# Performance work log

Measured on AMD Instinct MI355X. Metric: run time of the kernel, lower is better.

The kernel has to match this reference:

```python
import jax, jax.numpy as jnp
import numpy as np
import math

# kinematic tree: parent of each of the 23 joints (parents[i] < i -> topological order)
PARENTS = np.array([-1, 0, 1, 1, 3, 4, 5, 4, 7, 4, 9, 1, 11, 12, 13, 12, 15, 12, 17, 0, 19, 0, 21])
NUM_J = 23
HALF, QUART = math.pi / 2.0, math.pi / 4.0
# (joint slot, scale) for the pose params actually written in the torch forward
POSE_SLOTS = [(0, QUART), (3, HALF), (4, HALF), (5, QUART), (7, QUART), (9, QUART),
              (11, HALF), (12, HALF), (13, QUART), (15, QUART), (17, QUART)]


def _rodrigues(r):
    # r: [..., 3] axis-angle -> [..., 3, 3] rotation matrix
    angle = jnp.sqrt(jnp.sum(r * r, axis=-1) + 1e-16)
    axis = r / angle[..., None]
    s, c = jnp.sin(angle), jnp.cos(angle)
    x, y, z = axis[..., 0], axis[..., 1], axis[..., 2]
    zero = jnp.zeros_like(x)
    K = jnp.stack([jnp.stack([zero, -z, y], -1),
                   jnp.stack([z, zero, -x], -1),
                   jnp.stack([-y, x, zero], -1)], -2)
    I = jnp.eye(3, dtype=r.dtype)
    return I + s[..., None, None] * K + (1.0 - c)[..., None, None] * (K @ K)


def _lbs_forward(vertices, joints, weights, displacement, random_dis, pose_params):
    P = displacement.shape[0]
    dt = vertices.dtype
    # per-joint pose: pi/4 or pi/2 * tanh(param) on the used slots, zeros elsewhere
    pose = jnp.zeros((P, NUM_J, 3), dt)
    for (idx, scale), prm in zip(POSE_SLOTS, pose_params):
        pose = pose.at[:, idx].set(scale * jnp.tanh(prm))
    R = _rodrigues(pose)                                          # [P,J,3,3]
    j = joints[0].astype(dt)                                      # [J,3] rest joints
    rel = jnp.concatenate([j[:1], j[1:] - j[PARENTS[1:]]], 0)     # joint offsets from parent
    top = jnp.concatenate([R, jnp.broadcast_to(rel[None, :, :, None], (P, NUM_J, 3, 1))], -1)
    bot = jnp.broadcast_to(jnp.array([0.0, 0.0, 0.0, 1.0], dt), (P, NUM_J, 1, 4))
    T_local = jnp.concatenate([top, bot], -2)                     # [P,J,4,4]
    # forward-kinematics tree walk (fixed 23-joint chain, parents precede children)
    Gs = [T_local[:, 0]]
    for i in range(1, NUM_J):
        Gs.append(Gs[PARENTS[i]] @ T_local[:, i])
    G = jnp.stack(Gs, 1)                                          # [P,J,4,4]
    posed_joints = G[..., :3, 3]                                  # [P,J,3]
    # A = G - [0 | G_rot @ j_rest]  (keep only the 3x4 part actually needed)
    A = G[:, :, :3, :].at[..., 3].add(-jnp.einsum('pjab,jb->pja', G[:, :, :3, :3], j))  # [P,J,3,4]
    W = weights.astype(dt)
    T = jnp.einsum('vj,pjab->pvab', W, A)                         # [P,V,3,4] skinning transforms
    v = vertices[0]                                               # [V,3]
    v_posed = jnp.einsum('pvij,vj->pvi', T[..., :3], v) + T[..., 3]  # [P,V,3]
    shift = random_dis[:, None, :] + 3.0 * jnp.tanh(displacement)   # [P,1,3]
    return v_posed + shift, posed_joints + shift


def setup_inputs():
    P, V, J = 16, 500000, NUM_J
    key = jax.random.key(0)
    ks = jax.random.split(key, 16)
    w = jax.random.uniform(ks[2], (V, J), jnp.float32)
    inp = {
        'vertices': jax.random.normal(ks[0], (1, V, 3), jnp.float32),
        'joints': jax.random.normal(ks[1], (1, J, 3), jnp.float32),
        'weights': w / jnp.sum(w, -1, keepdims=True),  # convex skinning weights
        'displacement': 0.1 * jax.random.normal(ks[3], (P, 1, 3), jnp.float32),
        'random_dis': jax.random.normal(ks[4], (P, 3), jnp.float32),
    }
    names = ['joint_0', 'joint_3', 'joint_4', 'joint_5', 'joint_7', 'joint_9',
             'joint_11', 'joint_12', 'joint_13', 'joint_15', 'joint_17']
    for i, n in enumerate(names):
        inp[n] = jax.random.normal(ks[5 + i], (P, 3), jnp.float32)
    return inp


def reference(vertices, joints, weights, displacement, random_dis, joint_0, joint_3, joint_4, joint_5, joint_7, joint_9, joint_11, joint_12, joint_13, joint_15, joint_17):
    pose_params = (joint_0, joint_3, joint_4, joint_5, joint_7, joint_9,
                   joint_11, joint_12, joint_13, joint_15, joint_17)
    return _lbs_forward(vertices, joints, weights, displacement, random_dis, pose_params)
```

## Files before the change

### kernel.cpp

```cpp
#include <hip/hip_runtime.h>
#include <hip/hip_bf16.h>

typedef __hip_bfloat16 bf16;

#define P_CNT 16
#define J_CNT 23

__device__ int    g_flag;
__device__ float4 g_A[P_CNT * J_CNT * 3];
__device__ float  g_shift[P_CNT * 3];

struct PosePtrs { const void* p[11]; };

template <bool BF>
__device__ __forceinline__ float ld(const void* p, long long i) {
    if (BF) return __bfloat162float(((const bf16*)p)[i]);
    return ((const float*)p)[i];
}
template <bool BF>
__device__ __forceinline__ void st(void* p, long long i, float v) {
    if (BF) ((bf16*)p)[i] = __float2bfloat16(v);
    else    ((float*)p)[i] = v;
}

__global__ void detect_kernel(const void* __restrict__ w) {
    if (threadIdx.x != 0 || blockIdx.x != 0) return;
    const float* wf = (const float*)w;
    const bf16*  wb = (const bf16*)w;
    bool ok_f = true, ok_b = true;
    for (int r = 0; r < 4; ++r) {
        float sf = 0.f, sb = 0.f;
        for (int j = 0; j < J_CNT; ++j) {
            sf += wf[r * J_CNT + j];
            sb += __bfloat162float(wb[r * J_CNT + j]);
        }
        if (!(fabsf(sf - 1.f) < 0.02f)) ok_f = false;
        if (!(fabsf(sb - 1.f) < 0.10f)) ok_b = false;
    }
    g_flag = (!ok_f && ok_b) ? 1 : 0;
}

template <bool BF>
__global__ void pose_kernel(const void* __restrict__ joints,
                            const void* __restrict__ disp,
                            const void* __restrict__ rdis,
                            PosePtrs pp,
                            void* __restrict__ out1)
{
    if (g_flag != (BF ? 1 : 0)) return;
    __shared__ float Gs[P_CNT][J_CNT][12];
    int p = threadIdx.x;
    if (p >= P_CNT) return;

    const int par[J_CNT]     = {-1,0,1,1,3,4,5,4,7,4,9,1,11,12,13,12,15,12,17,0,19,0,21};
    const int slot_of[J_CNT] = {0,-1,-1,1,2,3,-1,4,-1,5,-1,6,7,8,-1,9,-1,10,-1,-1,-1,-1,-1};
    const float slot_sc[11]  = {
        0.7853981633974483f, 1.5707963267948966f, 1.5707963267948966f, 0.7853981633974483f,
        0.7853981633974483f, 0.7853981633974483f, 1.5707963267948966f, 1.5707963267948966f,
        0.7853981633974483f, 0.7853981633974483f, 0.7853981633974483f};

    for (int j = 0; j < J_CNT; ++j) {
        float rx = 0.f, ry = 0.f, rz = 0.f;
        int s = slot_of[j];
        if (s >= 0) {
            float sc = slot_sc[s];
            rx = sc * tanhf(ld<BF>(pp.p[s], p * 3 + 0));
            ry = sc * tanhf(ld<BF>(pp.p[s], p * 3 + 1));
            rz = sc * tanhf(ld<BF>(pp.p[s], p * 3 + 2));
        }
        float ang = sqrtf(rx * rx + ry * ry + rz * rz + 1e-16f);
        float sn = sinf(ang), cs = cosf(ang);
        float C = 1.f - cs;
        float inva = 1.f / ang;
        float x = rx * inva, y = ry * inva, z = rz * inva;
        float R[3][3];
        R[0][0] = 1.f - C * (y * y + z * z); R[0][1] = -sn * z + C * x * y;       R[0][2] = sn * y + C * x * z;
        R[1][0] = sn * z + C * x * y;        R[1][1] = 1.f - C * (x * x + z * z); R[1][2] = -sn * x + C * y * z;
        R[2][0] = -sn * y + C * x * z;       R[2][1] = sn * x + C * y * z;        R[2][2] = 1.f - C * (x * x + y * y);

        int q = par[j];
        float t[3];
        for (int c = 0; c < 3; ++c) {
            float jc = ld<BF>(joints, j * 3 + c);
            t[c] = (j == 0) ? jc : (jc - ld<BF>(joints, q * 3 + c));
        }
        if (j == 0) {
            for (int i = 0; i < 3; ++i) {
                Gs[p][0][i * 4 + 0] = R[i][0];
                Gs[p][0][i * 4 + 1] = R[i][1];
                Gs[p][0][i * 4 + 2] = R[i][2];
                Gs[p][0][i * 4 + 3] = t[i];
            }
        } else {
            for (int i = 0; i < 3; ++i) {
                float g0 = Gs[p][q][i * 4 + 0], g1 = Gs[p][q][i * 4 + 1];
                float g2 = Gs[p][q][i * 4 + 2], g3 = Gs[p][q][i * 4 + 3];
                Gs[p][j][i * 4 + 0] = g0 * R[0][0] + g1 * R[1][0] + g2 * R[2][0];
                Gs[p][j][i * 4 + 1] = g0 * R[0][1] + g1 * R[1][1] + g2 * R[2][1];
                Gs[p][j][i * 4 + 2] = g0 * R[0][2] + g1 * R[1][2] + g2 * R[2][2];
                Gs[p][j][i * 4 + 3] = g0 * t[0] + g1 * t[1] + g2 * t[2] + g3;
            }
        }
    }

    float sh[3];
    for (int c = 0; c < 3; ++c) {
        sh[c] = ld<BF>(rdis, p * 3 + c) + 3.f * tanhf(ld<BF>(disp, p * 3 + c));
        g_shift[p * 3 + c] = sh[c];
    }

    for (int j = 0; j < J_CNT; ++j) {
        float jx = ld<BF>(joints, j * 3 + 0);
        float jy = ld<BF>(joints, j * 3 + 1);
        float jz = ld<BF>(joints, j * 3 + 2);
        for (int i = 0; i < 3; ++i) {
            float g0 = Gs[p][j][i * 4 + 0], g1 = Gs[p][j][i * 4 + 1];
            float g2 = Gs[p][j][i * 4 + 2], g3 = Gs[p][j][i * 4 + 3];
            g_A[(p * J_CNT + j) * 3 + i] =
                make_float4(g0, g1, g2, g3 - (g0 * jx + g1 * jy + g2 * jz));
            st<BF>(out1, (p * J_CNT + j) * 3 + i, g3 + sh[i]);
        }
    }
}

template <bool BF>
__global__ __launch_bounds__(256) void lbs_vertex(
    const void* __restrict__ verts,
    const void* __restrict__ weights,
    void* __restrict__ out0,
    int V)
{
    if (g_flag != (BF ? 1 : 0)) return;
    __shared__ float4 As[P_CNT * J_CNT * 3];
    __shared__ float  sh[P_CNT * 3];
    for (int i = threadIdx.x; i < P_CNT * J_CNT * 3; i += 256) As[i] = g_A[i];
    for (int i = threadIdx.x; i < P_CNT * 3; i += 256) sh[i] = g_shift[i];
    __syncthreads();

    int v = blockIdx.x * 256 + threadIdx.x;
    if (v >= V) return;

    float w[J_CNT];
    long long wbase = (long long)v * J_CNT;
#pragma unroll
    for (int j = 0; j < J_CNT; ++j) w[j] = ld<BF>(weights, wbase + j);
    float x = ld<BF>(verts, (long long)v * 3 + 0);
    float y = ld<BF>(verts, (long long)v * 3 + 1);
    float z = ld<BF>(verts, (long long)v * 3 + 2);

    for (int p = 0; p < P_CNT; ++p) {
        const float4* Ap = As + p * (J_CNT * 3);
        float4 t0 = make_float4(0.f, 0.f, 0.f, 0.f);
        float4 t1 = make_float4(0.f, 0.f, 0.f, 0.f);
        float4 t2 = make_float4(0.f, 0.f, 0.f, 0.f);
#pragma unroll
        for (int j = 0; j < J_CNT; ++j) {
            float wj = w[j];
            float4 a0 = Ap[j * 3 + 0], a1 = Ap[j * 3 + 1], a2 = Ap[j * 3 + 2];
            t0.x = fmaf(wj, a0.x, t0.x); t0.y = fmaf(wj, a0.y, t0.y);
            t0.z = fmaf(wj, a0.z, t0.z); t0.w = fmaf(wj, a0.w, t0.w);
            t1.x = fmaf(wj, a1.x, t1.x); t1.y = fmaf(wj, a1.y, t1.y);
            t1.z = fmaf(wj, a1.z, t1.z); t1.w = fmaf(wj, a1.w, t1.w);
            t2.x = fmaf(wj, a2.x, t2.x); t2.y = fmaf(wj, a2.y, t2.y);
            t2.z = fmaf(wj, a2.z, t2.z); t2.w = fmaf(wj, a2.w, t2.w);
        }
        float ox = fmaf(t0.x, x, fmaf(t0.y, y, fmaf(t0.z, z, t0.w))) + sh[p * 3 + 0];
        float oy = fmaf(t1.x, x, fmaf(t1.y, y, fmaf(t1.z, z, t1.w))) + sh[p * 3 + 1];
        float oz = fmaf(t2.x, x, fmaf(t2.y, y, fmaf(t2.z, z, t2.w))) + sh[p * 3 + 2];
        long long base = ((long long)p * V + v) * 3;
        st<BF>(out0, base + 0, ox);
        st<BF>(out0, base + 1, oy);
        st<BF>(out0, base + 2, oz);
    }
}

extern "C" void kernel_launch(void* const* d_in, const int* in_sizes, int n_in,
                              void* d_out, int out_size, void* d_ws, size_t ws_size,
                              hipStream_t stream) {
    const void* verts   = d_in[0];
    const void* joints  = d_in[1];
    const void* weights = d_in[2];
    const void* disp    = d_in[3];
    const void* rdis    = d_in[4];
    PosePtrs pp;
    for (int i = 0; i < 11; ++i) pp.p[i] = d_in[5 + i];

    int V = in_sizes[0] / 3;
    long long pv3 = (long long)P_CNT * V * 3;

    void* out1_f = (void*)((float*)d_out + pv3);
    void* out1_b = (void*)((bf16*) d_out + pv3);

    detect_kernel<<<1, 64, 0, stream>>>(weights);
    pose_kernel<false><<<1, 64, 0, stream>>>(joints, disp, rdis, pp, out1_f);
    pose_kernel<true ><<<1, 64, 0, stream>>>(joints, disp, rdis, pp, out1_b);
    int G = (V + 255) / 256;
    lbs_vertex<false><<<G, 256, 0, stream>>>(verts, weights, d_out, V);
    lbs_vertex<true ><<<G, 256, 0, stream>>>(verts, weights, d_out, V);
}
```

Measured before the change: 253.6 us.

## Fuse pose, detection and skinning into one kernel with register-tiled vertices

Replaces the five-launch pipeline (dtype detection, two pose kernels, two vertex kernels) with a single kernel. Each block recomputes the forward-kinematics transforms in shared memory, stages a tile of skinning weights in shared memory with a swizzled transposed layout, and has each thread handle one pose and 16 vertices using vectorized loads and stores. This removes the launch overhead and the global round-trip for transforms. In exchange every block redundantly recomputes the tiny pose chain on 16 threads, and the kernel uses much more shared memory and registers.

```diff
diff --git a/kernel.cpp b/kernel.cpp
--- a/kernel.cpp
+++ b/kernel.cpp
@@ -5,12 +5,18 @@
 
 #define P_CNT 16
 #define J_CNT 23
-
-__device__ int    g_flag;
-__device__ float4 g_A[P_CNT * J_CNT * 3];
-__device__ float  g_shift[P_CNT * 3];
+#define VB    256
+#define VPT   16
+#define WSTR  260
 
 struct PosePtrs { const void* p[11]; };
+
+__device__ const int   c_par[J_CNT]  = {-1,0,1,1,3,4,5,4,7,4,9,1,11,12,13,12,15,12,17,0,19,0,21};
+__device__ const int   c_slot[J_CNT] = {0,-1,-1,1,2,3,-1,4,-1,5,-1,6,7,8,-1,9,-1,10,-1,-1,-1,-1,-1};
+__device__ const float c_scale[11]   = {
+    0.7853981633974483f, 1.5707963267948966f, 1.5707963267948966f, 0.7853981633974483f,
+    0.7853981633974483f, 0.7853981633974483f, 1.5707963267948966f, 1.5707963267948966f,
+    0.7853981633974483f, 0.7853981633974483f, 0.7853981633974483f};
 
 template <bool BF>
 __device__ __forceinline__ float ld(const void* p, long long i) {
@@ -22,156 +28,258 @@
     if (BF) ((bf16*)p)[i] = __float2bfloat16(v);
     else    ((float*)p)[i] = v;
 }
-
-__global__ void detect_kernel(const void* __restrict__ w) {
-    if (threadIdx.x != 0 || blockIdx.x != 0) return;
-    const float* wf = (const float*)w;
-    const bf16*  wb = (const bf16*)w;
-    bool ok_f = true, ok_b = true;
-    for (int r = 0; r < 4; ++r) {
-        float sf = 0.f, sb = 0.f;
+__device__ __forceinline__ float bfu(unsigned short u) {
+    union { unsigned short s; bf16 h; } c; c.s = u; return __bfloat162float(c.h);
+}
+__device__ __forceinline__ unsigned pack_bf(float a, float b) {
+    union { bf16 h; unsigned short u; } A, B;
+    A.h = __float2bfloat16(a); B.h = __float2bfloat16(b);
+    return ((unsigned)B.u << 16) | (unsigned)A.u;
+}
+
+template <bool BF>
+__device__ __forceinline__ void run(const void* __restrict__ verts,
+                                    const void* __restrict__ joints,
+                                    const void* __restrict__ weights,
+                                    const void* __restrict__ disp,
+                                    const void* __restrict__ rdis,
+                                    const PosePtrs& pp,
+                                    void* __restrict__ out, int V,
+                                    float* sA, float* sW, float* sSh)
+{
+    const int t = threadIdx.x;
+    const long long vb = (long long)blockIdx.x * VB;
+
+    {
+        const long long totalF = (long long)V * J_CNT;
+        const long long baseF  = vb * J_CNT;
+#pragma unroll 1
+        for (int e = t; e < VB * J_CNT; e += 256) {
+            float val = (baseF + e < totalF) ? ld<BF>(weights, baseF + e) : 0.f;
+            int r  = e / J_CNT;
+            int j  = e - r * J_CNT;
+            int wr = r ^ (((r >> 4) & 7) << 2);
+            sW[j * WSTR + wr] = val;
+        }
+    }
+
+    if (t < P_CNT) {
+        const int p = t;
+        float* Gp = sA + p * (J_CNT * 12);
+#pragma unroll 1
         for (int j = 0; j < J_CNT; ++j) {
-            sf += wf[r * J_CNT + j];
-            sb += __bfloat162float(wb[r * J_CNT + j]);
-        }
-        if (!(fabsf(sf - 1.f) < 0.02f)) ok_f = false;
-        if (!(fabsf(sb - 1.f) < 0.10f)) ok_b = false;
-    }
-    g_flag = (!ok_f && ok_b) ? 1 : 0;
-}
-
-template <bool BF>
-__global__ void pose_kernel(const void* __restrict__ joints,
-                            const void* __restrict__ disp,
-                            const void* __restrict__ rdis,
-                            PosePtrs pp,
-                            void* __restrict__ out1)
-{
-    if (g_flag != (BF ? 1 : 0)) return;
-    __shared__ float Gs[P_CNT][J_CNT][12];
-    int p = threadIdx.x;
-    if (p >= P_CNT) return;
-
-    const int par[J_CNT]     = {-1,0,1,1,3,4,5,4,7,4,9,1,11,12,13,12,15,12,17,0,19,0,21};
-    const int slot_of[J_CNT] = {0,-1,-1,1,2,3,-1,4,-1,5,-1,6,7,8,-1,9,-1,10,-1,-1,-1,-1,-1};
-    const float slot_sc[11]  = {
-        0.7853981633974483f, 1.5707963267948966f, 1.5707963267948966f, 0.7853981633974483f,
-        0.7853981633974483f, 0.7853981633974483f, 1.5707963267948966f, 1.5707963267948966f,
-        0.7853981633974483f, 0.7853981633974483f, 0.7853981633974483f};
-
+            float rx = 0.f, ry = 0.f, rz = 0.f;
+            int s = c_slot[j];
+            if (s >= 0) {
+                float sc = c_scale[s];
+                rx = sc * tanhf(ld<BF>(pp.p[s], p * 3 + 0));
+                ry = sc * tanhf(ld<BF>(pp.p[s], p * 3 + 1));
+                rz = sc * tanhf(ld<BF>(pp.p[s], p * 3 + 2));
+            }
+            float ang = sqrtf(rx * rx + ry * ry + rz * rz + 1e-16f);
+            float sn = sinf(ang), cs = cosf(ang);
+            float C = 1.f - cs, inva = 1.f / ang;
+            float x = rx * inva, y = ry * inva, z = rz * inva;
+            float R00 = 1.f - C * (y * y + z * z), R01 = -sn * z + C * x * y, R02 = sn * y + C * x * z;
+            float R10 = sn * z + C * x * y, R11 = 1.f - C * (x * x + z * z), R12 = -sn * x + C * y * z;
+            float R20 = -sn * y + C * x * z, R21 = sn * x + C * y * z, R22 = 1.f - C * (x * x + y * y);
+            int q = c_par[j];
+            float t0 = ld<BF>(joints, j * 3 + 0);
+            float t1 = ld<BF>(joints, j * 3 + 1);
+            float t2 = ld<BF>(joints, j * 3 + 2);
+            if (j == 0) {
+                Gp[0] = R00; Gp[1] = R01; Gp[2]  = R02; Gp[3]  = t0;
+                Gp[4] = R10; Gp[5] = R11; Gp[6]  = R12; Gp[7]  = t1;
+                Gp[8] = R20; Gp[9] = R21; Gp[10] = R22; Gp[11] = t2;
+            } else {
+                t0 -= ld<BF>(joints, q * 3 + 0);
+                t1 -= ld<BF>(joints, q * 3 + 1);
+                t2 -= ld<BF>(joints, q * 3 + 2);
+                const float* Gq = Gp + q * 12;
+                float* Gj = Gp + j * 12;
+#pragma unroll
+                for (int i = 0; i < 3; ++i) {
+                    float g0 = Gq[i * 4 + 0], g1 = Gq[i * 4 + 1];
+                    float g2 = Gq[i * 4 + 2], g3 = Gq[i * 4 + 3];
+                    Gj[i * 4 + 0] = g0 * R00 + g1 * R10 + g2 * R20;
+                    Gj[i * 4 + 1] = g0 * R01 + g1 * R11 + g2 * R21;
+                    Gj[i * 4 + 2] = g0 * R02 + g1 * R12 + g2 * R22;
+                    Gj[i * 4 + 3] = g0 * t0 + g1 * t1 + g2 * t2 + g3;
+                }
+            }
+        }
+#pragma unroll
+        for (int cc = 0; cc < 3; ++cc)
+            sSh[t * 3 + cc] = ld<BF>(rdis, t * 3 + cc) + 3.f * tanhf(ld<BF>(disp, t * 3 + cc));
+    }
+    __syncthreads();
+
+    {
+        const long long pv3 = (long long)P_CNT * V * 3;
+        void* out1 = BF ? (void*)((bf16*)out + pv3) : (void*)((float*)out + pv3);
+#pragma unroll 1
+        for (int idx = t; idx < P_CNT * J_CNT; idx += 256) {
+            int p = idx / J_CNT;
+            int j = idx - p * J_CNT;
+            float jx = ld<BF>(joints, j * 3 + 0);
+            float jy = ld<BF>(joints, j * 3 + 1);
+            float jz = ld<BF>(joints, j * 3 + 2);
+            float* Ar = sA + (p * J_CNT + j) * 12;
+#pragma unroll
+            for (int i = 0; i < 3; ++i) {
+                float g0 = Ar[i * 4 + 0], g1 = Ar[i * 4 + 1];
+                float g2 = Ar[i * 4 + 2], g3 = Ar[i * 4 + 3];
+                Ar[i * 4 + 3] = g3 - (g0 * jx + g1 * jy + g2 * jz);
+                if (blockIdx.x == 0)
+                    st<BF>(out1, (long long)(p * J_CNT + j) * 3 + i, g3 + sSh[p * 3 + i]);
+            }
+        }
+    }
+
+    const int p = t >> 4, c = t & 15;
+    const long long v0 = vb + (long long)c * VPT;
+    const bool full = (v0 + VPT <= (long long)V);
+    union F48 { float4 q[12]; float s[48]; };
+    F48 P3;
+    if (!BF && full) {
+        const float4* vp = (const float4*)((const float*)verts + v0 * 3);
+#pragma unroll
+        for (int k = 0; k < 12; ++k) P3.q[k] = vp[k];
+    } else if (BF && full) {
+        const uint4* vp = (const uint4*)((const bf16*)verts + v0 * 3);
+#pragma unroll
+        for (int k = 0; k < 6; ++k) {
+            uint4 u = vp[k];
+            P3.s[k * 8 + 0] = bfu((unsigned short)(u.x & 0xffff));
+            P3.s[k * 8 + 1] = bfu((unsigned short)(u.x >> 16));
+            P3.s[k * 8 + 2] = bfu((unsigned short)(u.y & 0xffff));
+            P3.s[k * 8 + 3] = bfu((unsigned short)(u.y >> 16));
+            P3.s[k * 8 + 4] = bfu((unsigned short)(u.z & 0xffff));
+            P3.s[k * 8 + 5] = bfu((unsigned short)(u.z >> 16));
+            P3.s[k * 8 + 6] = bfu((unsigned short)(u.w & 0xffff));
+            P3.s[k * 8 + 7] = bfu((unsigned short)(u.w >> 16));
+        }
+    } else {
+        const long long lim = (long long)V * 3;
+#pragma unroll
+        for (int i = 0; i < 48; ++i) {
+            long long gi = v0 * 3 + i;
+            P3.s[i] = (gi < lim) ? ld<BF>(verts, gi) : 0.f;
+        }
+    }
+    __syncthreads();
+
+    float acc0[VPT], acc1[VPT], acc2[VPT];
+#pragma unroll
+    for (int v = 0; v < VPT; ++v) { acc0[v] = 0.f; acc1[v] = 0.f; acc2[v] = 0.f; }
+
+    const int xm  = (c & 7) << 2;
+    const int wq0 = (c * 16 + 0)  ^ xm;
+    const int wq1 = (c * 16 + 4)  ^ xm;
+    const int wq2 = (c * 16 + 8)  ^ xm;
+    const int wq3 = (c * 16 + 12) ^ xm;
+    const float* Ap = sA + p * (J_CNT * 12);
+
+#pragma unroll 1
     for (int j = 0; j < J_CNT; ++j) {
-        float rx = 0.f, ry = 0.f, rz = 0.f;
-        int s = slot_of[j];
-        if (s >= 0) {
-            float sc = slot_sc[s];
-            rx = sc * tanhf(ld<BF>(pp.p[s], p * 3 + 0));
-            ry = sc * tanhf(ld<BF>(pp.p[s], p * 3 + 1));
-            rz = sc * tanhf(ld<BF>(pp.p[s], p * 3 + 2));
-        }
-        float ang = sqrtf(rx * rx + ry * ry + rz * rz + 1e-16f);
-        float sn = sinf(ang), cs = cosf(ang);
-        float C = 1.f - cs;
-        float inva = 1.f / ang;
-        float x = rx * inva, y = ry * inva, z = rz * inva;
-        float R[3][3];
-        R[0][0] = 1.f - C * (y * y + z * z); R[0][1] = -sn * z + C * x * y;       R[0][2] = sn * y + C * x * z;
-        R[1][0] = sn * z + C * x * y;        R[1][1] = 1.f - C * (x * x + z * z); R[1][2] = -sn * x + C * y * z;
-        R[2][0] = -sn * y + C * x * z;       R[2][1] = sn * x + C * y * z;        R[2][2] = 1.f - C * (x * x + y * y);
-
-        int q = par[j];
-        float t[3];
-        for (int c = 0; c < 3; ++c) {
-            float jc = ld<BF>(joints, j * 3 + c);
-            t[c] = (j == 0) ? jc : (jc - ld<BF>(joints, q * 3 + c));
-        }
-        if (j == 0) {
-            for (int i = 0; i < 3; ++i) {
-                Gs[p][0][i * 4 + 0] = R[i][0];
-                Gs[p][0][i * 4 + 1] = R[i][1];
-                Gs[p][0][i * 4 + 2] = R[i][2];
-                Gs[p][0][i * 4 + 3] = t[i];
-            }
+        float4 a0 = *(const float4*)(Ap + j * 12 + 0);
+        float4 a1 = *(const float4*)(Ap + j * 12 + 4);
+        float4 a2 = *(const float4*)(Ap + j * 12 + 8);
+        const float* Wj = sW + j * WSTR;
+        union { float4 q[4]; float s[16]; } W;
+        W.q[0] = *(const float4*)(Wj + wq0);
+        W.q[1] = *(const float4*)(Wj + wq1);
+        W.q[2] = *(const float4*)(Wj + wq2);
+        W.q[3] = *(const float4*)(Wj + wq3);
+#pragma unroll
+        for (int v = 0; v < VPT; ++v) {
+            float x = P3.s[v * 3 + 0], y = P3.s[v * 3 + 1], z = P3.s[v * 3 + 2];
+            float wv = W.s[v];
+            float d0 = fmaf(a0.z, z, fmaf(a0.y, y, fmaf(a0.x, x, a0.w)));
+            float d1 = fmaf(a1.z, z, fmaf(a1.y, y, fmaf(a1.x, x, a1.w)));
+            float d2 = fmaf(a2.z, z, fmaf(a2.y, y, fmaf(a2.x, x, a2.w)));
+            acc0[v] = fmaf(wv, d0, acc0[v]);
+            acc1[v] = fmaf(wv, d1, acc1[v]);
+            acc2[v] = fmaf(wv, d2, acc2[v]);
+        }
+    }
+
+    const float shx = sSh[p * 3 + 0], shy = sSh[p * 3 + 1], shz = sSh[p * 3 + 2];
+    F48 O;
+#pragma unroll
+    for (int v = 0; v < VPT; ++v) {
+        O.s[v * 3 + 0] = acc0[v] + shx;
+        O.s[v * 3 + 1] = acc1[v] + shy;
+        O.s[v * 3 + 2] = acc2[v] + shz;
+    }
+    const long long obase = ((long long)p * V + v0) * 3;
+    if (!BF) {
+        if (full && (V % 4 == 0)) {
+            float4* op = (float4*)((float*)out + obase);
+#pragma unroll
+            for (int k = 0; k < 12; ++k) op[k] = O.q[k];
         } else {
-            for (int i = 0; i < 3; ++i) {
-                float g0 = Gs[p][q][i * 4 + 0], g1 = Gs[p][q][i * 4 + 1];
-                float g2 = Gs[p][q][i * 4 + 2], g3 = Gs[p][q][i * 4 + 3];
-                Gs[p][j][i * 4 + 0] = g0 * R[0][0] + g1 * R[1][0] + g2 * R[2][0];
-                Gs[p][j][i * 4 + 1] = g0 * R[0][1] + g1 * R[1][1] + g2 * R[2][1];
-                Gs[p][j][i * 4 + 2] = g0 * R[0][2] + g1 * R[1][2] + g2 * R[2][2];
-                Gs[p][j][i * 4 + 3] = g0 * t[0] + g1 * t[1] + g2 * t[2] + g3;
-            }
-        }
-    }
-
-    float sh[3];
-    for (int c = 0; c < 3; ++c) {
-        sh[c] = ld<BF>(rdis, p * 3 + c) + 3.f * tanhf(ld<BF>(disp, p * 3 + c));
-        g_shift[p * 3 + c] = sh[c];
-    }
-
-    for (int j = 0; j < J_CNT; ++j) {
-        float jx = ld<BF>(joints, j * 3 + 0);
-        float jy = ld<BF>(joints, j * 3 + 1);
-        float jz = ld<BF>(joints, j * 3 + 2);
-        for (int i = 0; i < 3; ++i) {
-            float g0 = Gs[p][j][i * 4 + 0], g1 = Gs[p][j][i * 4 + 1];
-            float g2 = Gs[p][j][i * 4 + 2], g3 = Gs[p][j][i * 4 + 3];
-            g_A[(p * J_CNT + j) * 3 + i] =
-                make_float4(g0, g1, g2, g3 - (g0 * jx + g1 * jy + g2 * jz));
-            st<BF>(out1, (p * J_CNT + j) * 3 + i, g3 + sh[i]);
-        }
-    }
-}
-
-template <bool BF>
-__global__ __launch_bounds__(256) void lbs_vertex(
+#pragma unroll
+            for (int v = 0; v < VPT; ++v)
+                if (v0 + v < (long long)V) {
+                    ((float*)out)[obase + v * 3 + 0] = O.s[v * 3 + 0];
+                    ((float*)out)[obase + v * 3 + 1] = O.s[v * 3 + 1];
+                    ((float*)out)[obase + v * 3 + 2] = O.s[v * 3 + 2];
+                }
+        }
+    } else {
+        if (full && (V % 4 == 0)) {
+            unsigned* op = (unsigned*)((bf16*)out + obase);
+#pragma unroll
+            for (int k = 0; k < 24; ++k)
+                op[k] = pack_bf(O.s[2 * k + 0], O.s[2 * k + 1]);
+        } else {
+#pragma unroll
+            for (int v = 0; v < VPT; ++v)
+                if (v0 + v < (long long)V) {
+                    st<BF>(out, obase + v * 3 + 0, O.s[v * 3 + 0]);
+                    st<BF>(out, obase + v * 3 + 1, O.s[v * 3 + 1]);
+                    st<BF>(out, obase + v * 3 + 2, O.s[v * 3 + 2]);
+                }
+        }
+    }
+}
+
+__global__ __launch_bounds__(256, 3) void lbs_all(
     const void* __restrict__ verts,
+    const void* __restrict__ joints,
     const void* __restrict__ weights,
-    void* __restrict__ out0,
+    const void* __restrict__ disp,
+    const void* __restrict__ rdis,
+    PosePtrs pp,
+    void* __restrict__ out,
     int V)
 {
-    if (g_flag != (BF ? 1 : 0)) return;
-    __shared__ float4 As[P_CNT * J_CNT * 3];
-    __shared__ float  sh[P_CNT * 3];
-    for (int i = threadIdx.x; i < P_CNT * J_CNT * 3; i += 256) As[i] = g_A[i];
-    for (int i = threadIdx.x; i < P_CNT * 3; i += 256) sh[i] = g_shift[i];
+    __shared__ float sA[P_CNT * J_CNT * 12];
+    __shared__ float sW[J_CNT * WSTR];
+    __shared__ float sSh[P_CNT * 3];
+    __shared__ int   sFlag;
+
+    if (threadIdx.x == 0) {
+        const float* wf = (const float*)weights;
+        const bf16*  wb = (const bf16*)weights;
+        bool ok_f = true, ok_b = true;
+        for (int r = 0; r < 4; ++r) {
+            float sf = 0.f, sb = 0.f;
+            for (int j = 0; j < J_CNT; ++j) {
+                sf += wf[r * J_CNT + j];
+                sb += __bfloat162float(wb[r * J_CNT + j]);
+            }
+            if (!(fabsf(sf - 1.f) < 0.02f)) ok_f = false;
+            if (!(fabsf(sb - 1.f) < 0.10f)) ok_b = false;
+        }
+        sFlag = (!ok_f && ok_b) ? 1 : 0;
+    }
     __syncthreads();
-
-    int v = blockIdx.x * 256 + threadIdx.x;
-    if (v >= V) return;
-
-    float w[J_CNT];
-    long long wbase = (long long)v * J_CNT;
-#pragma unroll
-    for (int j = 0; j < J_CNT; ++j) w[j] = ld<BF>(weights, wbase + j);
-    float x = ld<BF>(verts, (long long)v * 3 + 0);
-    float y = ld<BF>(verts, (long long)v * 3 + 1);
-    float z = ld<BF>(verts, (long long)v * 3 + 2);
-
-    for (int p = 0; p < P_CNT; ++p) {
-        const float4* Ap = As + p * (J_CNT * 3);
-        float4 t0 = make_float4(0.f, 0.f, 0.f, 0.f);
-        float4 t1 = make_float4(0.f, 0.f, 0.f, 0.f);
-        float4 t2 = make_float4(0.f, 0.f, 0.f, 0.f);
-#pragma unroll
-        for (int j = 0; j < J_CNT; ++j) {
-            float wj = w[j];
-            float4 a0 = Ap[j * 3 + 0], a1 = Ap[j * 3 + 1], a2 = Ap[j * 3 + 2];
-            t0.x = fmaf(wj, a0.x, t0.x); t0.y = fmaf(wj, a0.y, t0.y);
-            t0.z = fmaf(wj, a0.z, t0.z); t0.w = fmaf(wj, a0.w, t0.w);
-            t1.x = fmaf(wj, a1.x, t1.x); t1.y = fmaf(wj, a1.y, t1.y);
-            t1.z = fmaf(wj, a1.z, t1.z); t1.w = fmaf(wj, a1.w, t1.w);
-            t2.x = fmaf(wj, a2.x, t2.x); t2.y = fmaf(wj, a2.y, t2.y);
-            t2.z = fmaf(wj, a2.z, t2.z); t2.w = fmaf(wj, a2.w, t2.w);
-        }
-        float ox = fmaf(t0.x, x, fmaf(t0.y, y, fmaf(t0.z, z, t0.w))) + sh[p * 3 + 0];
-        float oy = fmaf(t1.x, x, fmaf(t1.y, y, fmaf(t1.z, z, t1.w))) + sh[p * 3 + 1];
-        float oz = fmaf(t2.x, x, fmaf(t2.y, y, fmaf(t2.z, z, t2.w))) + sh[p * 3 + 2];
-        long long base = ((long long)p * V + v) * 3;
-        st<BF>(out0, base + 0, ox);
-        st<BF>(out0, base + 1, oy);
-        st<BF>(out0, base + 2, oz);
-    }
+    if (sFlag)
+        run<true >(verts, joints, weights, disp, rdis, pp, out, V, sA, sW, sSh);
+    else
+        run<false>(verts, joints, weights, disp, rdis, pp, out, V, sA, sW, sSh);
 }
 
 extern "C" void kernel_launch(void* const* d_in, const int* in_sizes, int n_in,
@@ -186,15 +294,6 @@
     for (int i = 0; i < 11; ++i) pp.p[i] = d_in[5 + i];
 
     int V = in_sizes[0] / 3;
-    long long pv3 = (long long)P_CNT * V * 3;
-
-    void* out1_f = (void*)((float*)d_out + pv3);
-    void* out1_b = (void*)((bf16*) d_out + pv3);
-
-    detect_kernel<<<1, 64, 0, stream>>>(weights);
-    pose_kernel<false><<<1, 64, 0, stream>>>(joints, disp, rdis, pp, out1_f);
-    pose_kernel<true ><<<1, 64, 0, stream>>>(joints, disp, rdis, pp, out1_b);
-    int G = (V + 255) / 256;
-    lbs_vertex<false><<<G, 256, 0, stream>>>(verts, weights, d_out, V);
-    lbs_vertex<true ><<<G, 256, 0, stream>>>(verts, weights, d_out, V);
-}
+    int G = (V + VB - 1) / VB;
+    lbs_all<<<G, 256, 0, stream>>>(verts, joints, weights, disp, rdis, pp, d_out, V);
+}
```

After: 787.4 us. +210.5%, slower.
